# Kernel tuning notes

Hardware: AMD Instinct MI355X
Metric: run time of the kernel (lower is better)

Reference implementation:

```python
import jax, jax.numpy as jnp
import numpy as np

B, T, D_IN, HID, NB, NCLS = 256, 512, 64, 64, 10, 2


def ferro_basis(x, centers, widths, coeffs):
    """KAN-style ferroelectric basis expansion.
    x: (N, in_dim); centers/widths: (num_basis,); coeffs: (in_dim, num_basis, out_dim)
    returns (N, out_dim).
    """
    phi = jnp.tanh((x[..., None] - centers) / widths)  # (N, in_dim, num_basis)
    return jnp.einsum('bik,iko->bo', phi, coeffs)


def setup_inputs() -> dict:
    key = jax.random.key(0)
    ks = jax.random.split(key, 8)
    sc = 1.0 / np.sqrt(D_IN * NB)
    inp = {
        'x': jax.random.normal(ks[0], (B, T, D_IN), dtype=jnp.float32),
        'lift_centers': jnp.linspace(-1.0, 1.0, NB, dtype=jnp.float32),
        'lift_widths': jnp.full((NB,), 0.5, dtype=jnp.float32),
        'lift_coeffs': jax.random.normal(ks[1], (D_IN, NB, HID), dtype=jnp.float32) * sc,
        'rnn_centers': jnp.linspace(-1.0, 1.0, NB, dtype=jnp.float32),
        'rnn_widths': jnp.full((NB,), 0.5, dtype=jnp.float32),
        'rnn_coeffs': jax.random.normal(ks[2], (HID, NB, HID), dtype=jnp.float32) * (1.0 / np.sqrt(HID * NB)),
        'head_centers': jnp.linspace(-1.0, 1.0, NB, dtype=jnp.float32),
        'head_widths': jnp.full((NB,), 0.5, dtype=jnp.float32),
        'head_coeffs': jax.random.normal(ks[3], (HID, NB, HID), dtype=jnp.float32) * (1.0 / np.sqrt(HID * NB)),
        'head_W': jax.random.normal(ks[4], (HID, NCLS), dtype=jnp.float32) * (1.0 / np.sqrt(HID)),
        'head_b': jnp.zeros((NCLS,), dtype=jnp.float32),
    }
    return inp


def reference(x, lift_centers, lift_widths, lift_coeffs,
              rnn_centers, rnn_widths, rnn_coeffs,
              head_centers, head_widths, head_coeffs,
              head_W, head_b):
    b, t, d = x.shape
    # NODE_Encoder: t = linspace(0, T, steps=1) -> single time point, so odeint
    # returns h0 unchanged; z_t == lift(x_t). Lift applied to every timestep
    # (as in the original per-t loop), vectorized over B*T.
    z = ferro_basis(x.reshape(b * t, d), lift_centers, lift_widths, lift_coeffs)
    z = z.reshape(b, t, -1)  # (B, T, HID)
    # FullyNonlinearKANCell: combined[:, :hidden] == x_phi, so h_t = sigmoid(input_basis(z_t));
    # the recurrence is degenerate and the final h depends only on the last timestep.
    h = jax.nn.sigmoid(ferro_basis(z[:, -1, :], rnn_centers, rnn_widths, rnn_coeffs))
    # dropout: eval mode -> identity
    phi = jax.nn.sigmoid(ferro_basis(h, head_centers, head_widths, head_coeffs))
    logits = phi @ head_W + head_b  # (B, num_classes)
    return logits
```

## Files before the change

### kernel.cpp

```cpp
#include <hip/hip_runtime.h>
#include <math.h>

#define BB    256
#define TT    512
#define DIN   64
#define HIDD  64
#define NBAS  10
#define NCLS  2

#define NTHR  512
#define NW    8
#define EPW   80
#define NF4   20

__device__ __forceinline__ float sigmoidf_(float v) {
    return 1.0f / (1.0f + expf(-v));
}

__global__ __launch_bounds__(NTHR, 2) void kan_fwd(
    const float* __restrict__ x,
    const float* __restrict__ lift_c, const float* __restrict__ lift_w, const float* __restrict__ lift_coef,
    const float* __restrict__ rnn_c,  const float* __restrict__ rnn_w,  const float* __restrict__ rnn_coef,
    const float* __restrict__ head_c, const float* __restrict__ head_w, const float* __restrict__ head_coef,
    const float* __restrict__ W, const float* __restrict__ bvec,
    float* __restrict__ out)
{
    const int b    = blockIdx.x;
    const int t    = threadIdx.x;
    const int l    = t & 63;
    const int w    = t >> 6;
    const int esub = l >> 4;
    const int og   = (l & 15) << 2;

    __shared__ float act[DIN];
    __shared__ __align__(16) float part[NW][DIN];

    const int i0 = (w << 3) + l / NBAS,        k0 = l % NBAS;
    const int i1 = (w << 3) + (64 + l) / NBAS, k1 = (64 + l) % NBAS;
    const bool ph1 = (l < (EPW - 64));

    const float* xb = x + ((size_t)b * TT + (TT - 1)) * DIN;
    const float x0 = xb[i0];
    const float x1 = ph1 ? xb[i1] : 0.0f;

    const float lc0 = lift_c[k0], lw0 = 1.0f / lift_w[k0];
    const float lc1 = lift_c[k1], lw1 = 1.0f / lift_w[k1];
    const float rc0 = rnn_c[k0],  rw0 = 1.0f / rnn_w[k0];
    const float rc1 = rnn_c[k1],  rw1 = 1.0f / rnn_w[k1];
    const float hc0 = head_c[k0], hw0 = 1.0f / head_w[k0];
    const float hc1 = head_c[k1], hw1 = 1.0f / head_w[k1];
    float W0 = 0.0f, W1 = 0.0f;
    if (t < DIN) { W0 = W[t * NCLS + 0]; W1 = W[t * NCLS + 1]; }

    const size_t fbase = (size_t)(EPW * w + esub) * 16 + (og >> 2);
    const float4* fA = (const float4*)lift_coef + fbase;
    const float4* fB = (const float4*)rnn_coef  + fbase;
    const float4* fC = (const float4*)head_coef + fbase;

    #define CONTRACT(ACC, PV0, PV1, CARR)                                       \
        {                                                                       \
            _Pragma("unroll")                                                   \
            for (int j = 0; j < NF4; ++j) {                                     \
                const float pj = (j < 16) ? __shfl((PV0), esub + 4 * j)         \
                                          : __shfl((PV1), esub + 4 * (j - 16)); \
                const float4 cf = (CARR)[j];                                    \
                (ACC).x = fmaf(pj, cf.x, (ACC).x);                              \
                (ACC).y = fmaf(pj, cf.y, (ACC).y);                              \
                (ACC).z = fmaf(pj, cf.z, (ACC).z);                              \
                (ACC).w = fmaf(pj, cf.w, (ACC).w);                              \
            }                                                                   \
        }

    #define XREDUCE(ACC)                                                        \
        {                                                                       \
            _Pragma("unroll")                                                   \
            for (int off = 16; off < 64; off <<= 1) {                           \
                (ACC).x += __shfl_xor((ACC).x, off);                            \
                (ACC).y += __shfl_xor((ACC).y, off);                            \
                (ACC).z += __shfl_xor((ACC).z, off);                            \
                (ACC).w += __shfl_xor((ACC).w, off);                            \
            }                                                                   \
        }

    float4 c1[NF4], c2[NF4];
    #pragma unroll
    for (int j = 0; j < NF4; ++j) c1[j] = fA[j * 64];
    #pragma unroll
    for (int j = 0; j < NF4; ++j) c2[j] = fB[j * 64];

    float pv0 = tanhf((x0 - lc0) * lw0);
    float pv1 = ph1 ? tanhf((x1 - lc1) * lw1) : 0.0f;

    float4 a = make_float4(0.f, 0.f, 0.f, 0.f);
    CONTRACT(a, pv0, pv1, c1);

    float4 c3[NF4];
    #pragma unroll
    for (int j = 0; j < NF4; ++j) c3[j] = fC[j * 64];

    XREDUCE(a);
    if (esub == 0) *(float4*)&part[w][og] = a;
    __syncthreads();
    if (t < DIN) {
        float s = 0.0f;
        #pragma unroll
        for (int ww = 0; ww < NW; ++ww) s += part[ww][t];
        act[t] = s;
    }
    __syncthreads();

    pv0 = tanhf((act[i0] - rc0) * rw0);
    pv1 = ph1 ? tanhf((act[i1] - rc1) * rw1) : 0.0f;

    a = make_float4(0.f, 0.f, 0.f, 0.f);
    CONTRACT(a, pv0, pv1, c2);
    XREDUCE(a);
    if (esub == 0) *(float4*)&part[w][og] = a;
    __syncthreads();
    if (t < DIN) {
        float s = 0.0f;
        #pragma unroll
        for (int ww = 0; ww < NW; ++ww) s += part[ww][t];
        act[t] = sigmoidf_(s);
    }
    __syncthreads();

    pv0 = tanhf((act[i0] - hc0) * hw0);
    pv1 = ph1 ? tanhf((act[i1] - hc1) * hw1) : 0.0f;

    a = make_float4(0.f, 0.f, 0.f, 0.f);
    CONTRACT(a, pv0, pv1, c3);
    XREDUCE(a);
    if (esub == 0) *(float4*)&part[w][og] = a;
    __syncthreads();

    if (t < DIN) {
        float s = 0.0f;
        #pragma unroll
        for (int ww = 0; ww < NW; ++ww) s += part[ww][t];
        s = sigmoidf_(s);
        float p0 = s * W0;
        float p1 = s * W1;
        #pragma unroll
        for (int off = 32; off > 0; off >>= 1) {
            p0 += __shfl_down(p0, off);
            p1 += __shfl_down(p1, off);
        }
        if (t == 0) {
            out[b * NCLS + 0] = p0 + bvec[0];
            out[b * NCLS + 1] = p1 + bvec[1];
        }
    }

    #undef CONTRACT
    #undef XREDUCE
}

extern "C" void kernel_launch(void* const* d_in, const int* in_sizes, int n_in,
                              void* d_out, int out_size, void* d_ws, size_t ws_size,
                              hipStream_t stream) {
    const float* x          = (const float*)d_in[0];
    const float* lift_c     = (const float*)d_in[1];
    const float* lift_w     = (const float*)d_in[2];
    const float* lift_coef  = (const float*)d_in[3];
    const float* rnn_c      = (const float*)d_in[4];
    const float* rnn_w      = (const float*)d_in[5];
    const float* rnn_coef   = (const float*)d_in[6];
    const float* head_c     = (const float*)d_in[7];
    const float* head_w     = (const float*)d_in[8];
    const float* head_coef  = (const float*)d_in[9];
    const float* W          = (const float*)d_in[10];
    const float* bvec       = (const float*)d_in[11];
    float* out              = (float*)d_out;

    kan_fwd<<<dim3(BB), dim3(NTHR), 0, stream>>>(
        x, lift_c, lift_w, lift_coef,
        rnn_c, rnn_w, rnn_coef,
        head_c, head_w, head_coef,
        W, bvec, out);
}
```

Measured before the change: 13.58 us.

## Double block to 1024 threads, halve per-warp basis elements, stagger coeff loads

Doubles the threads per block to 1024 (16 waves), so each wave handles 40 basis elements (4 input dims) instead of 80. The per-thread coefficient register arrays shrink from 20 to 10 float4s. Coefficient loads for the next stage are issued after the current contraction rather than all up front. The aim is more memory-level parallelism and lower register pressure. In exchange, the cross-wave reduction sums 16 partials, and all syncs span a larger block.

```diff
diff --git a/kernel.cpp b/kernel.cpp
--- a/kernel.cpp
+++ b/kernel.cpp
@@ -8,16 +8,16 @@
 #define NBAS  10
 #define NCLS  2
 
-#define NTHR  512
-#define NW    8
-#define EPW   80
-#define NF4   20
+#define NTHR  1024
+#define NW    16
+#define EPT   40
+#define NF4   10
 
 __device__ __forceinline__ float sigmoidf_(float v) {
     return 1.0f / (1.0f + expf(-v));
 }
 
-__global__ __launch_bounds__(NTHR, 2) void kan_fwd(
+__global__ __launch_bounds__(NTHR) void kan_fwd(
     const float* __restrict__ x,
     const float* __restrict__ lift_c, const float* __restrict__ lift_w, const float* __restrict__ lift_coef,
     const float* __restrict__ rnn_c,  const float* __restrict__ rnn_w,  const float* __restrict__ rnn_coef,
@@ -35,34 +35,26 @@
     __shared__ float act[DIN];
     __shared__ __align__(16) float part[NW][DIN];
 
-    const int i0 = (w << 3) + l / NBAS,        k0 = l % NBAS;
-    const int i1 = (w << 3) + (64 + l) / NBAS, k1 = (64 + l) % NBAS;
-    const bool ph1 = (l < (EPW - 64));
+    const bool pl  = (l < EPT);
+    const int  i0  = (w << 2) + l / NBAS;
+    const int  k0  = l % NBAS;
 
     const float* xb = x + ((size_t)b * TT + (TT - 1)) * DIN;
-    const float x0 = xb[i0];
-    const float x1 = ph1 ? xb[i1] : 0.0f;
+    const float x0 = pl ? xb[i0] : 0.0f;
 
-    const float lc0 = lift_c[k0], lw0 = 1.0f / lift_w[k0];
-    const float lc1 = lift_c[k1], lw1 = 1.0f / lift_w[k1];
-    const float rc0 = rnn_c[k0],  rw0 = 1.0f / rnn_w[k0];
-    const float rc1 = rnn_c[k1],  rw1 = 1.0f / rnn_w[k1];
-    const float hc0 = head_c[k0], hw0 = 1.0f / head_w[k0];
-    const float hc1 = head_c[k1], hw1 = 1.0f / head_w[k1];
     float W0 = 0.0f, W1 = 0.0f;
     if (t < DIN) { W0 = W[t * NCLS + 0]; W1 = W[t * NCLS + 1]; }
 
-    const size_t fbase = (size_t)(EPW * w + esub) * 16 + (og >> 2);
+    const size_t fbase = (size_t)(EPT * w + esub) * 16 + (og >> 2);
     const float4* fA = (const float4*)lift_coef + fbase;
     const float4* fB = (const float4*)rnn_coef  + fbase;
     const float4* fC = (const float4*)head_coef + fbase;
 
-    #define CONTRACT(ACC, PV0, PV1, CARR)                                       \
+    #define CONTRACT(ACC, PV, CARR)                                             \
         {                                                                       \
             _Pragma("unroll")                                                   \
             for (int j = 0; j < NF4; ++j) {                                     \
-                const float pj = (j < 16) ? __shfl((PV0), esub + 4 * j)         \
-                                          : __shfl((PV1), esub + 4 * (j - 16)); \
+                const float pj = __shfl((PV), esub + 4 * j);                    \
                 const float4 cf = (CARR)[j];                                    \
                 (ACC).x = fmaf(pj, cf.x, (ACC).x);                              \
                 (ACC).y = fmaf(pj, cf.y, (ACC).y);                              \
@@ -82,17 +74,34 @@
             }                                                                   \
         }
 
-    float4 c1[NF4], c2[NF4];
+    float4 c1[NF4];
     #pragma unroll
     for (int j = 0; j < NF4; ++j) c1[j] = fA[j * 64];
+
+    float pv = pl ? tanhf((x0 - lift_c[k0]) / lift_w[k0]) : 0.0f;
+
+    float4 a = make_float4(0.f, 0.f, 0.f, 0.f);
+    CONTRACT(a, pv, c1);
+
+    float4 c2[NF4];
     #pragma unroll
     for (int j = 0; j < NF4; ++j) c2[j] = fB[j * 64];
 
-    float pv0 = tanhf((x0 - lc0) * lw0);
-    float pv1 = ph1 ? tanhf((x1 - lc1) * lw1) : 0.0f;
+    XREDUCE(a);
+    if (esub == 0) *(float4*)&part[w][og] = a;
+    __syncthreads();
+    if (t < DIN) {
+        float s = 0.0f;
+        #pragma unroll
+        for (int ww = 0; ww < NW; ++ww) s += part[ww][t];
+        act[t] = s;
+    }
+    __syncthreads();
 
-    float4 a = make_float4(0.f, 0.f, 0.f, 0.f);
-    CONTRACT(a, pv0, pv1, c1);
+    pv = pl ? tanhf((act[i0] - rnn_c[k0]) / rnn_w[k0]) : 0.0f;
+
+    a = make_float4(0.f, 0.f, 0.f, 0.f);
+    CONTRACT(a, pv, c2);
 
     float4 c3[NF4];
     #pragma unroll
@@ -105,31 +114,14 @@
         float s = 0.0f;
         #pragma unroll
         for (int ww = 0; ww < NW; ++ww) s += part[ww][t];
-        act[t] = s;
-    }
-    __syncthreads();
-
-    pv0 = tanhf((act[i0] - rc0) * rw0);
-    pv1 = ph1 ? tanhf((act[i1] - rc1) * rw1) : 0.0f;
-
-    a = make_float4(0.f, 0.f, 0.f, 0.f);
-    CONTRACT(a, pv0, pv1, c2);
-    XREDUCE(a);
-    if (esub == 0) *(float4*)&part[w][og] = a;
-    __syncthreads();
-    if (t < DIN) {
-        float s = 0.0f;
-        #pragma unroll
-        for (int ww = 0; ww < NW; ++ww) s += part[ww][t];
         act[t] = sigmoidf_(s);
     }
     __syncthreads();
 
-    pv0 = tanhf((act[i0] - hc0) * hw0);
-    pv1 = ph1 ? tanhf((act[i1] - hc1) * hw1) : 0.0f;
+    pv = pl ? tanhf((act[i0] - head_c[k0]) / head_w[k0]) : 0.0f;
 
     a = make_float4(0.f, 0.f, 0.f, 0.f);
-    CONTRACT(a, pv0, pv1, c3);
+    CONTRACT(a, pv, c3);
     XREDUCE(a);
     if (esub == 0) *(float4*)&part[w][og] = a;
     __syncthreads();
```

Measured after the change: 12.57 us. 7.4% less time.
